# Kernel optimization log

Measured on AMD Instinct MI355X. Metric: run time of the kernel, lower is better.

## Reference

```python
import jax, jax.numpy as jnp
import numpy as np

EPS = 0.1          # GINConv init_eps (not learnable, learn_eps=False)
SLOPE = 0.01       # nn.LeakyReLU default negative_slope
NUM_NODES = 100000
NUM_EDGES = 3200000
NUM_GRAPHS = 100
D = 64
DIM1 = 64
R = 3
NUM_CLASSES = 10

def lrelu(v):
    return jax.nn.leaky_relu(v, negative_slope=SLOPE)

def setup_inputs() -> dict:
    key = jax.random.key(0)
    ks = jax.random.split(key, 20)
    inp = {
        "x": jax.random.normal(ks[0], (NUM_NODES, D), dtype=jnp.float32),
        "src": jax.random.randint(ks[1], (NUM_EDGES,), 0, NUM_NODES, dtype=jnp.int32),
        "dst": jax.random.randint(ks[2], (NUM_EDGES,), 0, NUM_NODES, dtype=jnp.int32),
        "graph_ids": jax.random.randint(ks[3], (NUM_NODES,), 0, NUM_GRAPHS, dtype=jnp.int32),
        "mlp0_W1": jax.random.normal(ks[4], (D, DIM1), dtype=jnp.float32) * 0.1,
        "mlp0_b1": jax.random.normal(ks[5], (DIM1,), dtype=jnp.float32) * 0.1,
        "mlp0_W2": jax.random.normal(ks[6], (DIM1, DIM1), dtype=jnp.float32) * 0.1,
        "mlp0_b2": jax.random.normal(ks[7], (DIM1,), dtype=jnp.float32) * 0.1,
        "mlps_W1": jax.random.normal(ks[8], (R - 1, DIM1, DIM1), dtype=jnp.float32) * 0.1,
        "mlps_b1": jax.random.normal(ks[9], (R - 1, DIM1), dtype=jnp.float32) * 0.1,
        "mlps_W2": jax.random.normal(ks[10], (R - 1, DIM1, DIM1), dtype=jnp.float32) * 0.1,
        "mlps_b2": jax.random.normal(ks[11], (R - 1, DIM1), dtype=jnp.float32) * 0.1,
        "cls_W1": jax.random.normal(ks[12], (DIM1, DIM1), dtype=jnp.float32) * 0.1,
        "cls_b1": jax.random.normal(ks[13], (DIM1,), dtype=jnp.float32) * 0.1,
        "cls_W2": jax.random.normal(ks[14], (DIM1, NUM_CLASSES), dtype=jnp.float32) * 0.1,
        "cls_b2": jax.random.normal(ks[15], (NUM_CLASSES,), dtype=jnp.float32) * 0.1,
    }
    return inp

def reference(x, src, dst, graph_ids, mlp0_W1, mlp0_b1, mlp0_W2, mlp0_b2,
              mlps_W1, mlps_b1, mlps_W2, mlps_b2, cls_W1, cls_b1, cls_W2, cls_b2):
    Y = x  # [N, d]
    for j in range(R):
        # GINConv 'sum': (1+eps)*h + sum over in-edges of neighbor features
        agg = jax.ops.segment_sum(Y[src], dst, num_segments=NUM_NODES)  # [N, f]
        h = (1.0 + EPS) * Y + agg
        if j == 0:
            W1, b1, W2, b2 = mlp0_W1, mlp0_b1, mlp0_W2, mlp0_b2
        else:
            W1, b1, W2, b2 = mlps_W1[j - 1], mlps_b1[j - 1], mlps_W2[j - 1], mlps_b2[j - 1]
        h = lrelu(h @ W1 + b1)
        h = lrelu(h @ W2 + b2)
        Y = lrelu(h)  # outer L_Relu in the source forward
    # per-graph sum readout, then classifier
    em = jax.ops.segment_sum(Y, graph_ids, num_segments=NUM_GRAPHS)  # [G, dim1]
    out = lrelu(em @ cls_W1 + cls_b1) @ cls_W2 + cls_b2  # [G, num_classes]
    return out
```

## Files before the change

kernel.cpp:

```cpp
#include <hip/hip_runtime.h>
#include <hip/hip_bf16.h>

#define N_NODES 100000
#define N_EDGES 3200000
#define N_GRAPHS 100
#define DIM 64
#define NCLS 10
#define EPS 0.1f
#define SLOPE 0.01f
#define TILES ((N_NODES + 255) / 256)
#define BIN_CH 8192
#define LDS_PAD 72
#define RO_BLOCKS 200

using half8  = __attribute__((ext_vector_type(8))) _Float16;
using half4v = __attribute__((ext_vector_type(4))) _Float16;
using f32x4  = __attribute__((ext_vector_type(4))) float;

__device__ __forceinline__ float lrelu(float v) {
    return v >= 0.f ? v : SLOPE * v;
}

__global__ void __launch_bounds__(256) bcount_kernel(const int* __restrict__ dst,
                                                     int* __restrict__ bsize, int E) {
    __shared__ int cnt[TILES];
    int t = threadIdx.x;
    for (int i = t; i < TILES; i += 256) cnt[i] = 0;
    __syncthreads();
    int e0 = blockIdx.x * BIN_CH;
    int e1 = e0 + BIN_CH; if (e1 > E) e1 = E;
    for (int e = e0 + t; e < e1; e += 256)
        atomicAdd(&cnt[(unsigned)dst[e] >> 8], 1);
    __syncthreads();
    for (int i = t; i < TILES; i += 256)
        if (cnt[i]) atomicAdd(&bsize[i], cnt[i]);
}

__global__ void __launch_bounds__(512) tile_scan_kernel(const int* __restrict__ tileSum,
                                                        int* __restrict__ tileBase,
                                                        int* __restrict__ bucketCur,
                                                        int* __restrict__ rowptr, int T) {
    __shared__ int sb[512];
    int t = threadIdx.x;
    int v = (t < T) ? tileSum[t] : 0;
    sb[t] = v;
    __syncthreads();
    for (int off = 1; off < 512; off <<= 1) {
        int u = (t >= off) ? sb[t - off] : 0;
        __syncthreads();
        sb[t] += u;
        __syncthreads();
    }
    if (t < T) {
        int base = sb[t] - v;
        tileBase[t]  = base;
        bucketCur[t] = base;
    }
    if (t == 511) rowptr[N_NODES] = sb[511];
}

__global__ void __launch_bounds__(256) binA_kernel(const int* __restrict__ src,
                                                   const int* __restrict__ dst,
                                                   int* __restrict__ bucketCur,
                                                   int* __restrict__ ssrcEnc, int E) {
    __shared__ int cnt[TILES];
    __shared__ int wbase[TILES];
    int t = threadIdx.x;
    for (int i = t; i < TILES; i += 256) cnt[i] = 0;
    __syncthreads();
    int e0 = blockIdx.x * BIN_CH;
    int e1 = e0 + BIN_CH; if (e1 > E) e1 = E;
    for (int e = e0 + t; e < e1; e += 256)
        atomicAdd(&cnt[(unsigned)dst[e] >> 8], 1);
    __syncthreads();
    for (int i = t; i < TILES; i += 256) {
        int c = cnt[i];
        wbase[i] = c ? atomicAdd(&bucketCur[i], c) : 0;
    }
    __syncthreads();
    for (int e = e0 + t; e < e1; e += 256) {
        int d = dst[e];
        int b = (unsigned)d >> 8;
        int p = atomicAdd(&wbase[b], 1);
        ssrcEnc[p] = (src[e] << 8) | (d & 255);
    }
}

__global__ void __launch_bounds__(256) binB_kernel(const int* __restrict__ ssrcEnc,
                                                   const int* __restrict__ tileBase,
                                                   int* __restrict__ rowptr,
                                                   int* __restrict__ ssrc, int E, int NB) {
    __shared__ int cnt[256];
    __shared__ int sb[256];
    __shared__ int cur[256];
    int b = blockIdx.x, t = threadIdx.x;
    cnt[t] = 0;
    __syncthreads();
    int base = tileBase[b];
    int endI = (b + 1 < NB) ? tileBase[b + 1] : E;
    for (int i = base + t; i < endI; i += 256)
        atomicAdd(&cnt[ssrcEnc[i] & 255], 1);
    __syncthreads();
    int v = cnt[t];
    sb[t] = v;
    __syncthreads();
    for (int off = 1; off < 256; off <<= 1) {
        int u = (t >= off) ? sb[t - off] : 0;
        __syncthreads();
        sb[t] += u;
        __syncthreads();
    }
    int node0 = b * 256;
    int nn = N_NODES - node0; if (nn > 256) nn = 256;
    if (t < nn) {
        int p = base + sb[t] - v;
        rowptr[node0 + t] = p;
        cur[t] = p;
    }
    __syncthreads();
    for (int i = base + t; i < endI; i += 256) {
        int enc = ssrcEnc[i];
        int p = atomicAdd(&cur[enc & 255], 1);
        ssrc[p] = enc >> 8;
    }
}

__global__ void __launch_bounds__(256) cvt_kernel(const float* __restrict__ x,
                                                  _Float16* __restrict__ H, int n4) {
    int i = blockIdx.x * 256 + threadIdx.x;
    if (i < n4) {
        float4 v = ((const float4*)x)[i];
        half4v h;
        h[0] = (_Float16)v.x; h[1] = (_Float16)v.y;
        h[2] = (_Float16)v.z; h[3] = (_Float16)v.w;
        ((half4v*)H)[i] = h;
    }
}

__global__ void __launch_bounds__(256) wcvt_kernel(const float* __restrict__ W0a,
                                                   const float* __restrict__ W0b,
                                                   const float* __restrict__ Ws1,
                                                   const float* __restrict__ Ws2,
                                                   _Float16* __restrict__ wfrag) {
    int f = blockIdx.x * 256 + threadIdx.x;
    if (f >= 6 * 4096) return;
    int i = f & 7, lane = (f >> 3) & 63, c = (f >> 9) & 3, k0 = (f >> 11) & 1, mat = f >> 12;
    int k = 32 * k0 + (lane >> 4) * 8 + i;
    int n = 16 * c + (lane & 15);
    const float* Wsrc;
    switch (mat) {
        case 0: Wsrc = W0a;        break;
        case 1: Wsrc = W0b;        break;
        case 2: Wsrc = Ws1;        break;
        case 3: Wsrc = Ws2;        break;
        case 4: Wsrc = Ws1 + 4096; break;
        default: Wsrc = Ws2 + 4096; break;
    }
    wfrag[f] = (_Float16)Wsrc[k * DIM + n];
}

__global__ void __launch_bounds__(256, 8) gather_kernel(const _Float16* __restrict__ H,
                                                        _Float16* __restrict__ aggH,
                                                        const int* __restrict__ rowptr,
                                                        const int* __restrict__ ssrc, int N) {
    const int tid = threadIdx.x, wave = tid >> 6, lane = tid & 63;
    const int g = lane >> 3, s = lane & 7;
    const int stride = gridDim.x * 4;
    const half8* __restrict__ Hv = (const half8*)H;
    for (int n = blockIdx.x * 4 + wave; n < N; n += stride) {
        int beg = rowptr[n], end = rowptr[n + 1];
        float a0[8], a1[8];
#pragma unroll
        for (int j = 0; j < 8; ++j) { a0[j] = 0.f; a1[j] = 0.f; }
        if (g == 0) {
            half8 v = Hv[(size_t)n * 8 + s];
#pragma unroll
            for (int j = 0; j < 8; ++j) a0[j] = (1.0f + EPS) * (float)v[j];
        }
        int e = beg + g;
        for (; e + 24 < end; e += 32) {
            int i0 = ssrc[e], i1 = ssrc[e + 8], i2 = ssrc[e + 16], i3 = ssrc[e + 24];
            half8 v0 = Hv[(size_t)i0 * 8 + s];
            half8 v1 = Hv[(size_t)i1 * 8 + s];
            half8 v2 = Hv[(size_t)i2 * 8 + s];
            half8 v3 = Hv[(size_t)i3 * 8 + s];
#pragma unroll
            for (int j = 0; j < 8; ++j) {
                a0[j] += (float)v0[j] + (float)v1[j];
                a1[j] += (float)v2[j] + (float)v3[j];
            }
        }
        for (; e + 8 < end; e += 16) {
            int i0 = ssrc[e], i1 = ssrc[e + 8];
            half8 v0 = Hv[(size_t)i0 * 8 + s];
            half8 v1 = Hv[(size_t)i1 * 8 + s];
#pragma unroll
            for (int j = 0; j < 8; ++j) { a0[j] += (float)v0[j]; a1[j] += (float)v1[j]; }
        }
        if (e < end) {
            int i0 = ssrc[e];
            half8 v0 = Hv[(size_t)i0 * 8 + s];
#pragma unroll
            for (int j = 0; j < 8; ++j) a0[j] += (float)v0[j];
        }
        half8 o;
#pragma unroll
        for (int j = 0; j < 8; ++j) {
            float f = a0[j] + a1[j];
            f += __shfl_xor(f, 8);
            f += __shfl_xor(f, 16);
            f += __shfl_xor(f, 32);
            o[j] = (_Float16)f;
        }
        if (g == 0)
            ((half8*)aggH)[(size_t)n * 8 + s] = o;
    }
}

__global__ void __launch_bounds__(256) mlp_mfma_kernel(
    const _Float16* __restrict__ aggH, _Float16* __restrict__ Hout,
    const _Float16* __restrict__ wf1, const _Float16* __restrict__ wf2,
    const float* __restrict__ b1, const float* __restrict__ b2, int nTiles) {
    __shared__ __align__(16) _Float16 sT[4][16 * LDS_PAD];
    const int tid = threadIdx.x, wave = tid >> 6, lane = tid & 63;
    const int lr = lane & 15;
    const int lg = lane >> 4;

    half8 B1[2][4], B2[2][4];
#pragma unroll
    for (int k0 = 0; k0 < 2; ++k0)
#pragma unroll
        for (int c = 0; c < 4; ++c) {
            B1[k0][c] = *(const half8*)(wf1 + ((k0 * 4 + c) * 64 + lane) * 8);
            B2[k0][c] = *(const half8*)(wf2 + ((k0 * 4 + c) * 64 + lane) * 8);
        }
    float b1c[4], b2c[4];
#pragma unroll
    for (int c = 0; c < 4; ++c) { b1c[c] = b1[16 * c + lr]; b2c[c] = b2[16 * c + lr]; }

    _Float16* myT = sT[wave];
    const int stride = gridDim.x * 4;
    for (int tile = blockIdx.x * 4 + wave; tile < nTiles; tile += stride) {
        const size_t row0 = (size_t)tile * 16;
        half8 A0 = *(const half8*)(aggH + (row0 + lr) * DIM + lg * 8);
        half8 A1 = *(const half8*)(aggH + (row0 + lr) * DIM + 32 + lg * 8);
        f32x4 acc[4];
#pragma unroll
        for (int c = 0; c < 4; ++c) {
            acc[c] = (f32x4){0.f, 0.f, 0.f, 0.f};
            acc[c] = __builtin_amdgcn_mfma_f32_16x16x32_f16(A0, B1[0][c], acc[c], 0, 0, 0);
            acc[c] = __builtin_amdgcn_mfma_f32_16x16x32_f16(A1, B1[1][c], acc[c], 0, 0, 0);
        }
#pragma unroll
        for (int c = 0; c < 4; ++c)
#pragma unroll
            for (int j = 0; j < 4; ++j)
                myT[(lg * 4 + j) * LDS_PAD + 16 * c + lr] =
                    (_Float16)lrelu(acc[c][j] + b1c[c]);
        half8 H0 = *(const half8*)(myT + lr * LDS_PAD + lg * 8);
        half8 H1 = *(const half8*)(myT + lr * LDS_PAD + 32 + lg * 8);
#pragma unroll
        for (int c = 0; c < 4; ++c) {
            acc[c] = (f32x4){0.f, 0.f, 0.f, 0.f};
            acc[c] = __builtin_amdgcn_mfma_f32_16x16x32_f16(H0, B2[0][c], acc[c], 0, 0, 0);
            acc[c] = __builtin_amdgcn_mfma_f32_16x16x32_f16(H1, B2[1][c], acc[c], 0, 0, 0);
        }
#pragma unroll
        for (int c = 0; c < 4; ++c)
#pragma unroll
            for (int j = 0; j < 4; ++j)
                myT[(lg * 4 + j) * LDS_PAD + 16 * c + lr] =
                    (_Float16)lrelu(lrelu(acc[c][j] + b2c[c]));
#pragma unroll
        for (int q = 0; q < 2; ++q) {
            half8 o = *(const half8*)(myT + lr * LDS_PAD + (lg + 4 * q) * 8);
            *(half8*)(Hout + (row0 + lr) * DIM + (lg + 4 * q) * 8) = o;
        }
    }
}

__global__ void __launch_bounds__(512) readout_f16_kernel(const _Float16* __restrict__ H,
                                                          const int* __restrict__ gid,
                                                          float* __restrict__ em, int N) {
    __shared__ float sAcc[N_GRAPHS * DIM];
    int tid = threadIdx.x;
    for (int i = tid; i < N_GRAPHS * DIM; i += 512) sAcc[i] = 0.f;
    __syncthreads();
    int lane = tid & 63, wave = tid >> 6;
    int chunk = (N + gridDim.x - 1) / gridDim.x;
    int beg = blockIdx.x * chunk;
    int end = beg + chunk; if (end > N) end = N;
    int n0 = beg + wave * 4;
    for (; n0 + 3 < end; n0 += 32) {
        int g0 = gid[n0], g1 = gid[n0 + 1], g2 = gid[n0 + 2], g3 = gid[n0 + 3];
        float v0 = (float)H[(size_t)(n0    ) * DIM + lane];
        float v1 = (float)H[(size_t)(n0 + 1) * DIM + lane];
        float v2 = (float)H[(size_t)(n0 + 2) * DIM + lane];
        float v3 = (float)H[(size_t)(n0 + 3) * DIM + lane];
        atomicAdd(&sAcc[g0 * DIM + lane], v0);
        atomicAdd(&sAcc[g1 * DIM + lane], v1);
        atomicAdd(&sAcc[g2 * DIM + lane], v2);
        atomicAdd(&sAcc[g3 * DIM + lane], v3);
    }
    for (int k = n0; k < end && k < n0 + 4; ++k) {
        int g = gid[k];
        atomicAdd(&sAcc[g * DIM + lane], (float)H[(size_t)k * DIM + lane]);
    }
    __syncthreads();
    for (int i = tid; i < N_GRAPHS * DIM; i += 512) atomicAdd(&em[i], sAcc[i]);
}

__global__ void __launch_bounds__(256) cls_kernel(const float* __restrict__ em,
                                                  const float* __restrict__ W1,
                                                  const float* __restrict__ b1,
                                                  const float* __restrict__ W2,
                                                  const float* __restrict__ b2,
                                                  float* __restrict__ out) {
    __shared__ float sT[N_GRAPHS * DIM];
    __shared__ float sW1[DIM * DIM];
    for (int i = threadIdx.x; i < DIM * DIM; i += 256) sW1[i] = W1[i];
    __syncthreads();
    for (int i = threadIdx.x; i < N_GRAPHS * DIM; i += 256) {
        int g = i >> 6, j = i & 63;
        float acc = b1[j];
#pragma unroll
        for (int k = 0; k < DIM; ++k) acc += em[g * DIM + k] * sW1[k * DIM + j];
        sT[i] = lrelu(acc);
    }
    __syncthreads();
    for (int i = threadIdx.x; i < N_GRAPHS * NCLS; i += 256) {
        int g = i / NCLS, c = i % NCLS;
        float acc = b2[c];
#pragma unroll
        for (int k = 0; k < DIM; ++k) acc += sT[g * DIM + k] * W2[k * NCLS + c];
        out[i] = acc;
    }
}

__global__ void copy_kernel(const float* __restrict__ x, float* __restrict__ Y, int n4) {
    int i = blockIdx.x * blockDim.x + threadIdx.x;
    if (i < n4) ((float4*)Y)[i] = ((const float4*)x)[i];
}

__global__ void __launch_bounds__(256) scatter_kernel(const float* __restrict__ Y,
                                                      const int* __restrict__ src,
                                                      const int* __restrict__ dst,
                                                      float* __restrict__ agg, int E) {
    int t = blockIdx.x * blockDim.x + threadIdx.x;
    int e = t >> 4;
    if (e >= E) return;
    int f4 = t & 15;
    int s = src[e];
    int d = dst[e];
    float4 v = ((const float4*)(Y + (size_t)s * DIM))[f4];
    float* ap = agg + (size_t)d * DIM + f4 * 4;
    atomicAdd(ap + 0, v.x);
    atomicAdd(ap + 1, v.y);
    atomicAdd(ap + 2, v.z);
    atomicAdd(ap + 3, v.w);
}

__global__ void __launch_bounds__(256) mlp_kernel(float* __restrict__ Y,
                                                  const float* __restrict__ agg,
                                                  const float* __restrict__ W1,
                                                  const float* __restrict__ b1,
                                                  const float* __restrict__ W2,
                                                  const float* __restrict__ b2, int N) {
    __shared__ float sW1[DIM * DIM];
    __shared__ float sW2[DIM * DIM];
    __shared__ float sb1[DIM];
    __shared__ float sb2[DIM];
    int tid = threadIdx.x;
    for (int i = tid; i < DIM * DIM; i += 256) { sW1[i] = W1[i]; sW2[i] = W2[i]; }
    if (tid < DIM) { sb1[tid] = b1[tid]; sb2[tid] = b2[tid]; }
    __syncthreads();
    int wave = tid >> 6, lane = tid & 63;
    int base = blockIdx.x * 64;
    for (int r = wave; r < 64; r += 4) {
        int row = base + r;
        if (row >= N) break;
        size_t off = (size_t)row * DIM + lane;
        float h = (1.0f + EPS) * Y[off] + agg[off];
        float acc = sb1[lane];
#pragma unroll
        for (int k = 0; k < DIM; ++k) acc += __shfl(h, k) * sW1[k * DIM + lane];
        acc = lrelu(acc);
        float acc2 = sb2[lane];
#pragma unroll
        for (int k = 0; k < DIM; ++k) acc2 += __shfl(acc, k) * sW2[k * DIM + lane];
        Y[off] = lrelu(lrelu(acc2));
    }
}

__global__ void __launch_bounds__(256) readout_kernel(const float* __restrict__ Y,
                                                      const int* __restrict__ gid,
                                                      float* __restrict__ em, int N) {
    __shared__ float sAcc[N_GRAPHS * DIM];
    for (int i = threadIdx.x; i < N_GRAPHS * DIM; i += 256) sAcc[i] = 0.f;
    __syncthreads();
    int lane = threadIdx.x & 63, wave = threadIdx.x >> 6;
    int stride = gridDim.x * 4;
    for (int n = blockIdx.x * 4 + wave; n < N; n += stride) {
        int g = gid[n];
        atomicAdd(&sAcc[g * DIM + lane], Y[(size_t)n * DIM + lane]);
    }
    __syncthreads();
    for (int i = threadIdx.x; i < N_GRAPHS * DIM; i += 256) atomicAdd(&em[i], sAcc[i]);
}

extern "C" void kernel_launch(void* const* d_in, const int* in_sizes, int n_in,
                              void* d_out, int out_size, void* d_ws, size_t ws_size,
                              hipStream_t stream) {
    const float* x       = (const float*)d_in[0];
    const int*   src     = (const int*)d_in[1];
    const int*   dst     = (const int*)d_in[2];
    const int*   gid     = (const int*)d_in[3];
    const float* mlp0_W1 = (const float*)d_in[4];
    const float* mlp0_b1 = (const float*)d_in[5];
    const float* mlp0_W2 = (const float*)d_in[6];
    const float* mlp0_b2 = (const float*)d_in[7];
    const float* mlps_W1 = (const float*)d_in[8];
    const float* mlps_b1 = (const float*)d_in[9];
    const float* mlps_W2 = (const float*)d_in[10];
    const float* mlps_b2 = (const float*)d_in[11];
    const float* cls_W1  = (const float*)d_in[12];
    const float* cls_b1  = (const float*)d_in[13];
    const float* cls_W2  = (const float*)d_in[14];
    const float* cls_b2  = (const float*)d_in[15];
    float* out = (float*)d_out;

    const size_t szH  = (size_t)N_NODES * DIM * sizeof(_Float16);
    const size_t szY  = (size_t)N_NODES * DIM * sizeof(float);
    const size_t szEm = (size_t)N_GRAPHS * DIM * sizeof(float);
    const size_t szRp = (size_t)(N_NODES + 16) * sizeof(int);
    const size_t szE  = (size_t)N_EDGES * sizeof(int);
    const size_t szT  = 512 * sizeof(int);
    const size_t szWf = 6 * 4096 * sizeof(_Float16);
    const size_t need = 4 * szH + szE + szEm + szRp + 3 * szT + szWf;

    const float* roundB1[3] = {mlp0_b1, mlps_b1, mlps_b1 + DIM};
    const float* roundB2[3] = {mlp0_b2, mlps_b2, mlps_b2 + DIM};

    if (ws_size >= need) {
        char* w = (char*)d_ws;
        char* slabU   = w;                w += szH;
        _Float16* Ha  = (_Float16*)w;     w += szH;
        _Float16* Hb  = (_Float16*)w;     w += szH;
        _Float16* aggH= (_Float16*)w;     w += szH;
        int*  ssrc    = (int*)w;          w += szE;
        float* em     = (float*)w;        w += szEm;
        int*  rowptr  = (int*)w;          w += szRp;
        int*  tileS   = (int*)w;          w += szT;
        int*  tileB   = (int*)w;          w += szT;
        int*  bCur    = (int*)w;          w += szT;
        _Float16* wfrag = (_Float16*)w;   w += szWf;
        int*      ssrcEnc = (int*)slabU;
        _Float16* Hx      = (_Float16*)slabU;

        hipMemsetAsync(tileS, 0, szT, stream);
        int aBlocks = (N_EDGES + BIN_CH - 1) / BIN_CH;
        bcount_kernel<<<aBlocks, 256, 0, stream>>>(dst, tileS, N_EDGES);
        tile_scan_kernel<<<1, 512, 0, stream>>>(tileS, tileB, bCur, rowptr, TILES);
        binA_kernel<<<aBlocks, 256, 0, stream>>>(src, dst, bCur, ssrcEnc, N_EDGES);
        binB_kernel<<<TILES, 256, 0, stream>>>(ssrcEnc, tileB, rowptr, ssrc, N_EDGES, TILES);

        wcvt_kernel<<<96, 256, 0, stream>>>(mlp0_W1, mlp0_W2, mlps_W1, mlps_W2, wfrag);

        int n4 = N_NODES * DIM / 4;
        cvt_kernel<<<(n4 + 255) / 256, 256, 0, stream>>>(x, Hx, n4);

        const _Float16* Hin[3]  = {Hx, Ha, Hb};
        _Float16*       Hout[3] = {Ha, Hb, Ha};
        const int nTiles = N_NODES / 16;
        const int mBlocks = (nTiles + 3) / 4;
        for (int j = 0; j < 3; ++j) {
            gather_kernel<<<2048, 256, 0, stream>>>(Hin[j], aggH, rowptr, ssrc, N_NODES);
            mlp_mfma_kernel<<<mBlocks, 256, 0, stream>>>(aggH, Hout[j],
                                                         wfrag + (size_t)(2 * j) * 4096,
                                                         wfrag + (size_t)(2 * j + 1) * 4096,
                                                         roundB1[j], roundB2[j], nTiles);
        }

        hipMemsetAsync(em, 0, szEm, stream);
        readout_f16_kernel<<<RO_BLOCKS, 512, 0, stream>>>(Ha, gid, em, N_NODES);
        cls_kernel<<<1, 256, 0, stream>>>(em, cls_W1, cls_b1, cls_W2, cls_b2, out);
    } else {
        const float* roundW1[3] = {mlp0_W1, mlps_W1, mlps_W1 + DIM * DIM};
        const float* roundW2[3] = {mlp0_W2, mlps_W2, mlps_W2 + DIM * DIM};
        float* Y   = (float*)d_ws;
        float* agg = Y + (size_t)N_NODES * DIM;
        float* em  = agg + (size_t)N_NODES * DIM;
        int n4 = N_NODES * DIM / 4;
        copy_kernel<<<(n4 + 255) / 256, 256, 0, stream>>>(x, Y, n4);
        for (int j = 0; j < 3; ++j) {
            hipMemsetAsync(agg, 0, szY, stream);
            long long threads = (long long)N_EDGES * 16;
            int blocks = (int)((threads + 255) / 256);
            scatter_kernel<<<blocks, 256, 0, stream>>>(Y, src, dst, agg, N_EDGES);
            int mb = (N_NODES + 63) / 64;
            mlp_kernel<<<mb, 256, 0, stream>>>(Y, agg, roundW1[j], roundB1[j],
                                               roundW2[j], roundB2[j], N_NODES);
        }
        hipMemsetAsync(em, 0, szEm, stream);
        readout_kernel<<<128, 256, 0, stream>>>(Y, gid, em, N_NODES);
        cls_kernel<<<1, 256, 0, stream>>>(em, cls_W1, cls_b1, cls_W2, cls_b2, out);
    }
}
```

Baseline: 364.7 us.

## Stage edge binning in LDS and coarsen destination buckets to 512 nodes

The first-pass edge binning kernel now sorts its chunk of encoded edges into an LDS buffer by bucket, using a local prefix scan. Each wave then copies whole bucket runs to global memory contiguously, replacing scattered per-edge writes with mostly coalesced ones. Buckets grow from 256 to 512 nodes, which halves the bucket count so the local scan fits in one 256-thread block, and the second-pass kernel moves to 512 threads. The costs are more LDS per block (lower occupancy) and extra scan and synchronisation overhead in the binning kernel.

```diff
diff --git a/kernel.cpp b/kernel.cpp
--- a/kernel.cpp
+++ b/kernel.cpp
@@ -8,7 +8,9 @@
 #define NCLS 10
 #define EPS 0.1f
 #define SLOPE 0.01f
-#define TILES ((N_NODES + 255) / 256)
+#define BUCKET 512
+#define BUCKET_SH 9
+#define NBKT ((N_NODES + BUCKET - 1) / BUCKET)
 #define BIN_CH 8192
 #define LDS_PAD 72
 #define RO_BLOCKS 200
@@ -23,16 +25,16 @@
 
 __global__ void __launch_bounds__(256) bcount_kernel(const int* __restrict__ dst,
                                                      int* __restrict__ bsize, int E) {
-    __shared__ int cnt[TILES];
+    __shared__ int cnt[NBKT];
     int t = threadIdx.x;
-    for (int i = t; i < TILES; i += 256) cnt[i] = 0;
+    for (int i = t; i < NBKT; i += 256) cnt[i] = 0;
     __syncthreads();
     int e0 = blockIdx.x * BIN_CH;
     int e1 = e0 + BIN_CH; if (e1 > E) e1 = E;
     for (int e = e0 + t; e < e1; e += 256)
-        atomicAdd(&cnt[(unsigned)dst[e] >> 8], 1);
-    __syncthreads();
-    for (int i = t; i < TILES; i += 256)
+        atomicAdd(&cnt[(unsigned)dst[e] >> BUCKET_SH], 1);
+    __syncthreads();
+    for (int i = t; i < NBKT; i += 256)
         if (cnt[i]) atomicAdd(&bsize[i], cnt[i]);
 }
 
@@ -63,65 +65,86 @@
                                                    const int* __restrict__ dst,
                                                    int* __restrict__ bucketCur,
                                                    int* __restrict__ ssrcEnc, int E) {
-    __shared__ int cnt[TILES];
-    __shared__ int wbase[TILES];
-    int t = threadIdx.x;
-    for (int i = t; i < TILES; i += 256) cnt[i] = 0;
+    __shared__ int ebuf[BIN_CH];
+    __shared__ int cnt[NBKT];
+    __shared__ int lbase[NBKT];
+    __shared__ int wbase[NBKT];
+    __shared__ int lcur[NBKT];
+    __shared__ int sscan[256];
+    const int t = threadIdx.x, wave = t >> 6, lane = t & 63;
+    for (int i = t; i < NBKT; i += 256) cnt[i] = 0;
     __syncthreads();
     int e0 = blockIdx.x * BIN_CH;
     int e1 = e0 + BIN_CH; if (e1 > E) e1 = E;
     for (int e = e0 + t; e < e1; e += 256)
-        atomicAdd(&cnt[(unsigned)dst[e] >> 8], 1);
-    __syncthreads();
-    for (int i = t; i < TILES; i += 256) {
-        int c = cnt[i];
-        wbase[i] = c ? atomicAdd(&bucketCur[i], c) : 0;
+        atomicAdd(&cnt[(unsigned)dst[e] >> BUCKET_SH], 1);
+    __syncthreads();
+    int v = (t < NBKT) ? cnt[t] : 0;
+    sscan[t] = v;
+    __syncthreads();
+    for (int off = 1; off < 256; off <<= 1) {
+        int u = (t >= off) ? sscan[t - off] : 0;
+        __syncthreads();
+        sscan[t] += u;
+        __syncthreads();
+    }
+    if (t < NBKT) {
+        int lb = sscan[t] - v;
+        lbase[t] = lb;
+        lcur[t]  = lb;
+        wbase[t] = v ? atomicAdd(&bucketCur[t], v) : 0;
     }
     __syncthreads();
     for (int e = e0 + t; e < e1; e += 256) {
         int d = dst[e];
-        int b = (unsigned)d >> 8;
-        int p = atomicAdd(&wbase[b], 1);
-        ssrcEnc[p] = (src[e] << 8) | (d & 255);
-    }
-}
-
-__global__ void __launch_bounds__(256) binB_kernel(const int* __restrict__ ssrcEnc,
+        int b = (unsigned)d >> BUCKET_SH;
+        int p = atomicAdd(&lcur[b], 1);
+        ebuf[p] = (src[e] << BUCKET_SH) | (d & (BUCKET - 1));
+    }
+    __syncthreads();
+    for (int b = wave; b < NBKT; b += 4) {
+        int c = cnt[b], lb = lbase[b], wb = wbase[b];
+        for (int k = lane; k < c; k += 64)
+            ssrcEnc[wb + k] = ebuf[lb + k];
+    }
+}
+
+__global__ void __launch_bounds__(512) binB_kernel(const int* __restrict__ ssrcEnc,
                                                    const int* __restrict__ tileBase,
                                                    int* __restrict__ rowptr,
                                                    int* __restrict__ ssrc, int E, int NB) {
-    __shared__ int cnt[256];
-    __shared__ int sb[256];
-    __shared__ int cur[256];
+    __shared__ int cnt[BUCKET];
+    __shared__ int sb[BUCKET];
+    __shared__ int cur[BUCKET];
     int b = blockIdx.x, t = threadIdx.x;
     cnt[t] = 0;
     __syncthreads();
     int base = tileBase[b];
     int endI = (b + 1 < NB) ? tileBase[b + 1] : E;
-    for (int i = base + t; i < endI; i += 256)
-        atomicAdd(&cnt[ssrcEnc[i] & 255], 1);
+    for (int i = base + t; i < endI; i += 512)
+        atomicAdd(&cnt[ssrcEnc[i] & (BUCKET - 1)], 1);
     __syncthreads();
     int v = cnt[t];
     sb[t] = v;
     __syncthreads();
-    for (int off = 1; off < 256; off <<= 1) {
+    for (int off = 1; off < 512; off <<= 1) {
         int u = (t >= off) ? sb[t - off] : 0;
         __syncthreads();
         sb[t] += u;
         __syncthreads();
     }
-    int node0 = b * 256;
-    int nn = N_NODES - node0; if (nn > 256) nn = 256;
+    int node0 = b * BUCKET;
+    int nn = N_NODES - node0; if (nn > BUCKET) nn = BUCKET;
     if (t < nn) {
         int p = base + sb[t] - v;
         rowptr[node0 + t] = p;
         cur[t] = p;
     }
     __syncthreads();
-    for (int i = base + t; i < endI; i += 256) {
+    for (int i = base + t; i < endI; i += 512) {
         int enc = ssrcEnc[i];
-        int p = atomicAdd(&cur[enc & 255], 1);
-        ssrc[p] = enc >> 8;
+        int p = atomicAdd(&cur[enc & (BUCKET - 1)], 1);
+        ssrc[p] = enc >> BUCKET_SH;
     }
 }
 
@@ -460,9 +483,9 @@
         hipMemsetAsync(tileS, 0, szT, stream);
         int aBlocks = (N_EDGES + BIN_CH - 1) / BIN_CH;
         bcount_kernel<<<aBlocks, 256, 0, stream>>>(dst, tileS, N_EDGES);
-        tile_scan_kernel<<<1, 512, 0, stream>>>(tileS, tileB, bCur, rowptr, TILES);
+        tile_scan_kernel<<<1, 512, 0, stream>>>(tileS, tileB, bCur, rowptr, NBKT);
         binA_kernel<<<aBlocks, 256, 0, stream>>>(src, dst, bCur, ssrcEnc, N_EDGES);
-        binB_kernel<<<TILES, 256, 0, stream>>>(ssrcEnc, tileB, rowptr, ssrc, N_EDGES, TILES);
+        binB_kernel<<<NBKT, 512, 0, stream>>>(ssrcEnc, tileB, rowptr, ssrc, N_EDGES, NBKT);
 
         wcvt_kernel<<<96, 256, 0, stream>>>(mlp0_W1, mlp0_W2, mlps_W1, mlps_W2, wfrag);
 
```

Result: no change. 370.5 us (+1.6%).
